# Kernel optimization log

Hardware: AMD Instinct MI355X
Metric: run time of the kernel (lower is better)

## Reference

```python
import jax, jax.numpy as jnp
import numpy as np

D_MODEL = 1024
N_HEADS = 16
N_PHASE = 128              # 8 * n_heads
PHASE_PER_HEAD = N_PHASE // N_HEADS   # 8
HEAD_DIM = D_MODEL // N_HEADS         # 64
B, L = 2, 2048
SCALE = 1.0 / np.sqrt(PHASE_PER_HEAD)
LN_EPS = 1e-5


def _pos_phase(seq_len, n_phase, base=10000.0):
    # RoPE-style frequencies; even and odd columns both carry sinusoid
    inv_freq = 1.0 / base ** (jnp.arange(0, n_phase, 2, dtype=jnp.float32) / n_phase)
    sinusoid = jnp.arange(seq_len, dtype=jnp.float32)[:, None] * inv_freq[None, :]  # (L, n_phase//2)
    return jnp.repeat(sinusoid, 2, axis=1)  # (L, n_phase): cols 0::2 and 1::2 equal sinusoid


def setup_inputs() -> dict:
    key = jax.random.key(0)
    ks = jax.random.split(key, 10)
    xavier = lambda k, shp: jax.random.normal(k, shp, jnp.float32) * np.sqrt(2.0 / (shp[0] + shp[1]))
    return {
        "x_real": jax.random.normal(ks[0], (B, L, D_MODEL), jnp.float32),
        "x_imag": jax.random.normal(ks[1], (B, L, D_MODEL), jnp.float32),
        "Wq": xavier(ks[2], (N_PHASE, D_MODEL)),
        "bq": jax.random.uniform(ks[3], (N_PHASE,), jnp.float32, -np.pi, np.pi),
        "Wk": xavier(ks[4], (N_PHASE, D_MODEL)),
        "bk": jax.random.uniform(ks[5], (N_PHASE,), jnp.float32, -np.pi, np.pi),
        "Wv": xavier(ks[6], (D_MODEL, D_MODEL)),
        "Wo": xavier(ks[7], (D_MODEL, D_MODEL)) / np.sqrt(2.0),
        "gamma": jnp.ones((D_MODEL,), jnp.float32),
        "beta": jnp.zeros((D_MODEL,), jnp.float32),
    }


def reference(x_real, x_imag, Wq, bq, Wk, bk, Wv, Wo, gamma, beta):
    b, l, d = x_real.shape
    pos = _pos_phase(l, N_PHASE)  # (L, n_phase), constant buffer

    # additive phase with position injection
    Qt = (x_imag @ Wq.T + bq + pos).reshape(b, l, N_HEADS, PHASE_PER_HEAD).transpose(0, 2, 1, 3)
    Kt = (x_imag @ Wk.T + bk + pos).reshape(b, l, N_HEADS, PHASE_PER_HEAD).transpose(0, 2, 1, 3)

    # cos(Qi)cos(Kj) + sin(Qi)sin(Kj) as one contraction over stacked features
    qf = jnp.concatenate([jnp.cos(Qt), jnp.sin(Qt)], axis=-1)  # (B,H,L,2P)
    kf = jnp.concatenate([jnp.cos(Kt), jnp.sin(Kt)], axis=-1)
    scores = jnp.einsum('bhip,bhjp->bhij', qf, kf) * SCALE     # (B,H,L,L)

    causal = jnp.triu(jnp.ones((l, l), dtype=bool), 1)
    scores = jnp.where(causal, -jnp.inf, scores)
    attn = jax.nn.softmax(scores, axis=-1)

    V = (x_real @ Wv.T).reshape(b, l, N_HEADS, HEAD_DIM).transpose(0, 2, 1, 3)  # (B,H,L,hd)
    out = jnp.einsum('bhij,bhjd->bhid', attn, V)
    out = out.transpose(0, 2, 1, 3).reshape(b, l, d) @ Wo.T

    # residual + LayerNorm (eps matches torch default)
    h = x_real + out
    mu = jnp.mean(h, axis=-1, keepdims=True)
    var = jnp.mean(jnp.square(h - mu), axis=-1, keepdims=True)
    out_real = (h - mu) * jax.lax.rsqrt(var + LN_EPS) * gamma + beta
    return (out_real, x_imag)
```

## Files before the change

### kernel.cpp

```cpp
#include <hip/hip_runtime.h>
#include <math.h>

#define D_MODEL 1024
#define N_HEADS 16
#define N_PHASE 128
#define HEAD_DIM 64
#define B_SZ 2
#define L_SEQ 2048
#define QK_SCALE 0.35355339059327373f
#define LN_EPS 1e-5f
#define POS_COEF 0.07195578415606394f
#define INV_2PI 0.15915494309189535f

typedef __attribute__((ext_vector_type(8))) short bf16x8;
typedef __attribute__((ext_vector_type(4))) short s16x4;
typedef __attribute__((ext_vector_type(4))) float f32x4;

__device__ __forceinline__ float wave_reduce_sum(float v) {
#pragma unroll
  for (int off = 32; off > 0; off >>= 1) v += __shfl_xor(v, off);
  return v;
}
__device__ __forceinline__ unsigned short f2bf(float x) {
  unsigned u = __float_as_uint(x);
  u += 0x7fffu + ((u >> 16) & 1u);
  return (unsigned short)(u >> 16);
}
__device__ __forceinline__ void gload16(const short* g, short* l) {
  __builtin_amdgcn_global_load_lds(
      (const __attribute__((address_space(1))) void*)g,
      (__attribute__((address_space(3))) void*)l, 16, 0, 0);
}
__device__ __forceinline__ void fast_sincos(float ang, float* s, float* c) {
  float rev = ang * INV_2PI;
  rev = rev - rintf(rev);
  *c = __builtin_amdgcn_cosf(rev);
  *s = __builtin_amdgcn_sinf(rev);
}

#define NX4 ((B_SZ * L_SEQ * D_MODEL) / 4)
#define NWP4 ((N_PHASE * D_MODEL) / 4)
#define NW4 ((D_MODEL * D_MODEL) / 4)
__device__ __forceinline__ s16x4 cvt4(float4 v) {
  s16x4 o;
  o[0] = (short)f2bf(v.x);
  o[1] = (short)f2bf(v.y);
  o[2] = (short)f2bf(v.z);
  o[3] = (short)f2bf(v.w);
  return o;
}
__global__ __launch_bounds__(256) void cvtall_kernel(
    const float* __restrict__ x_real, const float* __restrict__ x_imag,
    const float* __restrict__ Wq, const float* __restrict__ Wk,
    const float* __restrict__ Wv, const float* __restrict__ Wo,
    short* __restrict__ xr_bf, short* __restrict__ xi_bf,
    short* __restrict__ Wq_bf, short* __restrict__ Wk_bf,
    short* __restrict__ Wv_bf, short* __restrict__ Wo_bf,
    float* __restrict__ outi) {
  const int i = blockIdx.x * 256 + threadIdx.x;
  if (i < NX4) {
    const float4 vi = ((const float4*)x_imag)[i];
    ((float4*)outi)[i] = vi;
    ((s16x4*)xi_bf)[i] = cvt4(vi);
    ((s16x4*)xr_bf)[i] = cvt4(((const float4*)x_real)[i]);
  } else if (i < NX4 + NWP4) {
    const int j = i - NX4;
    ((s16x4*)Wq_bf)[j] = cvt4(((const float4*)Wq)[j]);
    ((s16x4*)Wk_bf)[j] = cvt4(((const float4*)Wk)[j]);
  } else if (i < NX4 + NWP4 + NW4) {
    const int j = i - NX4 - NWP4;
    ((s16x4*)Wv_bf)[j] = cvt4(((const float4*)Wv)[j]);
    ((s16x4*)Wo_bf)[j] = cvt4(((const float4*)Wo)[j]);
  }
}

__device__ __forceinline__ void gemm_core(const short* __restrict__ A,
                                          const short* __restrict__ Bm, int K,
                                          int mBase, int nBase,
                                          f32x4 acc[4][2], short* As,
                                          short* Bs) {
  const int tid = threadIdx.x;
  const int wv = tid >> 6, ln = tid & 63;
  const int wr = wv >> 1, wc = wv & 1;
  const int fr = ln & 15, fc = ln >> 4;
  const int cg = (ln & 3) ^ ((ln >> 3) & 3);
  const short* ga = A + (size_t)(mBase + wv * 16 + (ln >> 2)) * K + cg * 8;
  const short* gb = Bm + (size_t)(nBase + wv * 16 + (ln >> 2)) * K + cg * 8;
  short* la = As + wv * 512;
  short* lb = Bs + wv * 512;
  const int ra = (wr * 64 + fr) * 32 + (fc ^ ((fr >> 1) & 3)) * 8;
  const int rb = (wc * 32 + fr) * 32 + (fc ^ ((fr >> 1) & 3)) * 8;

  for (int k0 = 0; k0 < K; k0 += 32) {
    __syncthreads();
    gload16(ga + k0, la);
    gload16(ga + k0 + (size_t)64 * K, la + 64 * 32);
    gload16(gb + k0, lb);
    __syncthreads();

    bf16x8 af[4], bfr[2];
#pragma unroll
    for (int mi = 0; mi < 4; ++mi) af[mi] = *(const bf16x8*)&As[ra + mi * 512];
#pragma unroll
    for (int ni = 0; ni < 2; ++ni) bfr[ni] = *(const bf16x8*)&Bs[rb + ni * 512];

#pragma unroll
    for (int mi = 0; mi < 4; ++mi)
#pragma unroll
      for (int ni = 0; ni < 2; ++ni)
        acc[mi][ni] = __builtin_amdgcn_mfma_f32_16x16x32_bf16(
            af[mi], bfr[ni], acc[mi][ni], 0, 0, 0);
  }
}

__global__ __launch_bounds__(256) void qkv_kernel(
    const short* __restrict__ xi, const short* __restrict__ xr,
    const short* __restrict__ WqB, const short* __restrict__ WkB,
    const short* __restrict__ WvB, const float* __restrict__ bq,
    const float* __restrict__ bk, short* __restrict__ qf,
    short* __restrict__ kf, short* __restrict__ Vt) {
  __shared__ short As[128 * 32];
  __shared__ short Bs[64 * 32];
  const int y = blockIdx.y;
  const int mBase = blockIdx.x * 128;
  const short* A;
  const short* Bm;
  int nBase;
  if (y < 4) {
    A = xi;
    Bm = (y < 2) ? WqB : WkB;
    nBase = (y & 1) * 64;
  } else {
    A = xr;
    Bm = WvB;
    nBase = (y - 4) * 64;
  }

  f32x4 acc[4][2];
#pragma unroll
  for (int i = 0; i < 4; ++i)
#pragma unroll
    for (int j = 0; j < 2; ++j) acc[i][j] = (f32x4){0.f, 0.f, 0.f, 0.f};
  gemm_core(A, Bm, D_MODEL, mBase, nBase, acc, As, Bs);

  const int ln = threadIdx.x & 63, wv = threadIdx.x >> 6;
  const int wr = wv >> 1, wc = wv & 1;
  const int fr = ln & 15, fc = ln >> 4;

  if (y < 4) {
    const float* bias = (y < 2) ? bq : bk;
    short* Cs = (y < 2) ? qf : kf;
    const float fscale = (y < 2) ? QK_SCALE : 1.0f;
#pragma unroll
    for (int mi = 0; mi < 4; ++mi)
#pragma unroll
      for (int ni = 0; ni < 2; ++ni)
#pragma unroll
        for (int r = 0; r < 4; ++r) {
          const int m = mBase + wr * 64 + mi * 16 + fc * 4 + r;
          const int n = nBase + wc * 32 + ni * 16 + fr;
          const int b = m >> 11, l = m & (L_SEQ - 1);
          const float inv_freq = __expf(-(float)(n & ~1) * POS_COEF);
          const float ang = acc[mi][ni][r] + bias[n] + (float)l * inv_freq;
          float sv, cv;
          fast_sincos(ang, &sv, &cv);
          const int h = n >> 3, p = n & 7;
          const size_t base = ((size_t)((b << 4) + h) * L_SEQ + l) * 16;
          Cs[base + p] = (short)f2bf(cv * fscale);
          Cs[base + 8 + p] = (short)f2bf(sv * fscale);
        }
  } else {
#pragma unroll
    for (int mi = 0; mi < 4; ++mi)
#pragma unroll
      for (int ni = 0; ni < 2; ++ni) {
        const int n = nBase + wc * 32 + ni * 16 + fr;
        const int m = mBase + wr * 64 + mi * 16 + fc * 4;
        const int b = m >> 11, l = m & (L_SEQ - 1);
        const int t = (l >> 2) & 7;
        const int tp = ((t << 1) & 6) | (t >> 2);
        const int lpos = (l & ~31) | (tp << 2);
        const int h = n >> 6, d = n & 63;
        const int jc = lpos >> 5, jlo = lpos & 31;
        const int gg = jlo >> 3, ee = jlo & 7;
        s16x4 pk;
#pragma unroll
        for (int r = 0; r < 4; ++r) pk[r] = (short)f2bf(acc[mi][ni][r]);
        const size_t off = (size_t)((b << 4) + h) * 64 * L_SEQ +
                           (size_t)(jc * 4 + (d >> 4)) * 512 + gg * 128 +
                           (d & 15) * 8 + ee;
        *(s16x4*)&Vt[off] = pk;
      }
  }
}

__global__ __launch_bounds__(256) void ogemm_kernel(
    const short* __restrict__ A, const short* __restrict__ Bm,
    const float* __restrict__ resid, float* __restrict__ Cf) {
  __shared__ short As[128 * 32];
  __shared__ short Bs[64 * 32];
  const int mBase = blockIdx.x * 128, nBase = blockIdx.y * 64;

  f32x4 acc[4][2];
#pragma unroll
  for (int i = 0; i < 4; ++i)
#pragma unroll
    for (int j = 0; j < 2; ++j) acc[i][j] = (f32x4){0.f, 0.f, 0.f, 0.f};
  gemm_core(A, Bm, D_MODEL, mBase, nBase, acc, As, Bs);

  const int ln = threadIdx.x & 63, wv = threadIdx.x >> 6;
  const int wr = wv >> 1, wc = wv & 1;
  const int fr = ln & 15, fc = ln >> 4;
#pragma unroll
  for (int mi = 0; mi < 4; ++mi)
#pragma unroll
    for (int ni = 0; ni < 2; ++ni)
#pragma unroll
      for (int r = 0; r < 4; ++r) {
        const int m = mBase + wr * 64 + mi * 16 + fc * 4 + r;
        const int n = nBase + wc * 32 + ni * 16 + fr;
        const size_t idx = (size_t)m * D_MODEL + n;
        Cf[idx] = acc[mi][ni][r] + resid[idx];
      }
}

__global__ __launch_bounds__(256) void attn_mfma_kernel(
    const short* __restrict__ qf, const short* __restrict__ kf,
    const short* __restrict__ Vt, short* __restrict__ ao) {
  const int bh = blockIdx.x;
  const int qg = 127 - (int)blockIdx.y;
  const int tid = threadIdx.x;
  const int w = tid >> 6;
  const int lane = tid & 63;
  const int g = lane >> 4;
  const int q16 = lane & 15;
  const int qglob = qg * 16 + q16;
  const int ntiles = (qg >> 2) + 1;

  __shared__ float ol[4][16][68];
  __shared__ float ll[4][16];

  const short* qf_h = qf + (size_t)bh * L_SEQ * 16;
  const short* kf_h = kf + (size_t)bh * L_SEQ * 16;
  const short* Vt_h = Vt + (size_t)bh * 64 * L_SEQ;
  const int b = bh >> 4, h = bh & 15;

  bf16x8 qfrag = {0, 0, 0, 0, 0, 0, 0, 0};
  if (g < 2) qfrag = *(const bf16x8*)(qf_h + (size_t)qglob * 16 + g * 8);

  f32x4 o[4];
#pragma unroll
  for (int dc = 0; dc < 4; ++dc) o[dc] = (f32x4){0.f, 0.f, 0.f, 0.f};
  float lsum = 0.f;

#pragma unroll 1
  for (int t = w; t < ntiles; t += 4) {
    const int j0 = t << 6;

    bf16x8 vf0[4], vf1[4];
#pragma unroll
    for (int dc = 0; dc < 4; ++dc)
      vf0[dc] = *(const bf16x8*)(Vt_h + ((size_t)((2 * t) * 4 + dc) << 9) +
                                 lane * 8);

    bf16x8 kfr[4];
#pragma unroll
    for (int jt = 0; jt < 4; ++jt) {
      kfr[jt] = (bf16x8){0, 0, 0, 0, 0, 0, 0, 0};
      if (g < 2)
        kfr[jt] =
            *(const bf16x8*)(kf_h + (size_t)(j0 + jt * 16 + q16) * 16 + g * 8);
    }

    f32x4 s[4];
#pragma unroll
    for (int jt = 0; jt < 4; ++jt)
      s[jt] = __builtin_amdgcn_mfma_f32_16x16x32_bf16(
          kfr[jt], qfrag, (f32x4){0.f, 0.f, 0.f, 0.f}, 0, 0, 0);

#pragma unroll
    for (int dc = 0; dc < 4; ++dc)
      vf1[dc] = *(const bf16x8*)(Vt_h + ((size_t)((2 * t + 1) * 4 + dc) << 9) +
                                 lane * 8);

    if (t == ntiles - 1) {
#pragma unroll
      for (int jt = 0; jt < 4; ++jt)
#pragma unroll
        for (int r = 0; r < 4; ++r)
          if (j0 + jt * 16 + g * 4 + r > qglob) s[jt][r] = -INFINITY;
    }

    float ex[4][4];
#pragma unroll
    for (int jt = 0; jt < 4; ++jt)
#pragma unroll
      for (int r = 0; r < 4; ++r) {
        ex[jt][r] = __expf(s[jt][r]);
        lsum += ex[jt][r];
      }

#pragma unroll
    for (int c = 0; c < 2; ++c) {
      union {
        unsigned u[4];
        bf16x8 v;
      } pb;
#pragma unroll
      for (int hw = 0; hw < 2; ++hw) {
        asm("v_cvt_pk_bf16_f32 %0, %1, %2"
            : "=v"(pb.u[hw * 2 + 0])
            : "v"(ex[2 * c + hw][0]), "v"(ex[2 * c + hw][1]));
        asm("v_cvt_pk_bf16_f32 %0, %1, %2"
            : "=v"(pb.u[hw * 2 + 1])
            : "v"(ex[2 * c + hw][2]), "v"(ex[2 * c + hw][3]));
      }
      const bf16x8* vfc = c ? vf1 : vf0;
#pragma unroll
      for (int dc = 0; dc < 4; ++dc)
        o[dc] = __builtin_amdgcn_mfma_f32_16x16x32_bf16(vfc[dc], pb.v, o[dc],
                                                        0, 0, 0);
    }
  }

  lsum += __shfl_xor(lsum, 16);
  lsum += __shfl_xor(lsum, 32);
  if (g == 0) ll[w][q16] = lsum;
#pragma unroll
  for (int dc = 0; dc < 4; ++dc)
    *(f32x4*)&ol[w][q16][dc * 16 + g * 4] = o[dc];
  __syncthreads();

  const float lt = (ll[0][q16] + ll[1][q16]) + (ll[2][q16] + ll[3][q16]);
  const float inv = 1.f / lt;
  const int d0 = w * 16 + g * 4;
  s16x4 pk;
#pragma unroll
  for (int r = 0; r < 4; ++r) {
    const float v = ((ol[0][q16][d0 + r] + ol[1][q16][d0 + r]) +
                     (ol[2][q16][d0 + r] + ol[3][q16][d0 + r]));
    pk[r] = (short)f2bf(v * inv);
  }
  short* orow = ao + ((size_t)(b * L_SEQ + qglob)) * D_MODEL + h * 64;
  *(s16x4*)&orow[d0] = pk;
}

__global__ __launch_bounds__(256) void ln_kernel(float* __restrict__ io,
                                                 const float* __restrict__ gamma,
                                                 const float* __restrict__ beta) {
  const int row = blockIdx.x;
  float* p = io + (size_t)row * D_MODEL;
  const int tid = threadIdx.x;
  float4 x = ((const float4*)p)[tid];
  float s = x.x + x.y + x.z + x.w;
  float sq = x.x * x.x + x.y * x.y + x.z * x.z + x.w * x.w;
  s = wave_reduce_sum(s);
  sq = wave_reduce_sum(sq);
  __shared__ float ss[4], ssq[4];
  const int w = tid >> 6, lane = tid & 63;
  if (lane == 0) {
    ss[w] = s;
    ssq[w] = sq;
  }
  __syncthreads();
  s = ss[0] + ss[1] + ss[2] + ss[3];
  sq = ssq[0] + ssq[1] + ssq[2] + ssq[3];
  const float mean = s * (1.f / D_MODEL);
  const float var = sq * (1.f / D_MODEL) - mean * mean;
  const float rstd = rsqrtf(var + LN_EPS);
  const float4 g = ((const float4*)gamma)[tid];
  const float4 bt = ((const float4*)beta)[tid];
  float4 y;
  y.x = (x.x - mean) * rstd * g.x + bt.x;
  y.y = (x.y - mean) * rstd * g.y + bt.y;
  y.z = (x.z - mean) * rstd * g.z + bt.z;
  y.w = (x.w - mean) * rstd * g.w + bt.w;
  ((float4*)p)[tid] = y;
}

extern "C" void kernel_launch(void* const* d_in, const int* in_sizes, int n_in,
                              void* d_out, int out_size, void* d_ws,
                              size_t ws_size, hipStream_t stream) {
  const float* x_real = (const float*)d_in[0];
  const float* x_imag = (const float*)d_in[1];
  const float* Wq = (const float*)d_in[2];
  const float* bq = (const float*)d_in[3];
  const float* Wk = (const float*)d_in[4];
  const float* bk = (const float*)d_in[5];
  const float* Wv = (const float*)d_in[6];
  const float* Wo = (const float*)d_in[7];
  const float* gamma = (const float*)d_in[8];
  const float* beta = (const float*)d_in[9];

  const size_t n_x = (size_t)B_SZ * L_SEQ * D_MODEL;
  const size_t n_w = (size_t)D_MODEL * D_MODEL;
  const size_t n_wp = (size_t)N_PHASE * D_MODEL;
  const size_t n_qf = (size_t)B_SZ * N_HEADS * L_SEQ * 16;

  short* xi_bf = (short*)d_ws;
  short* xr_bf = xi_bf + n_x;
  short* Wq_bf = xr_bf + n_x;
  short* Wk_bf = Wq_bf + n_wp;
  short* Wv_bf = Wk_bf + n_wp;
  short* Wo_bf = Wv_bf + n_w;
  short* qf = Wo_bf + n_w;
  short* kf = qf + n_qf;
  short* Vt = kf + n_qf;
  short* ao_bf = xr_bf;

  float* outr = (float*)d_out;
  float* outi = outr + n_x;

  const dim3 blk(256);
  const int M = B_SZ * L_SEQ;

  const int cvt_blocks = (NX4 + NWP4 + NW4 + 255) / 256;
  cvtall_kernel<<<dim3(cvt_blocks), blk, 0, stream>>>(
      x_real, x_imag, Wq, Wk, Wv, Wo, xr_bf, xi_bf, Wq_bf, Wk_bf, Wv_bf,
      Wo_bf, outi);

  qkv_kernel<<<dim3(M / 128, 20), blk, 0, stream>>>(
      xi_bf, xr_bf, Wq_bf, Wk_bf, Wv_bf, bq, bk, qf, kf, Vt);
  attn_mfma_kernel<<<dim3(B_SZ * N_HEADS, 128), blk, 0, stream>>>(qf, kf, Vt,
                                                                  ao_bf);
  ogemm_kernel<<<dim3(M / 128, D_MODEL / 64), blk, 0, stream>>>(
      ao_bf, Wo_bf, x_real, outr);
  ln_kernel<<<dim3(M), blk, 0, stream>>>(outr, gamma, beta);
}
```

Baseline: 98.23 us.

## Double the GEMM K-tile to 64 and prefetch next attention tile's K/V

```diff
diff --git a/kernel.cpp b/kernel.cpp
--- a/kernel.cpp
+++ b/kernel.cpp
@@ -83,33 +83,45 @@
   const int wv = tid >> 6, ln = tid & 63;
   const int wr = wv >> 1, wc = wv & 1;
   const int fr = ln & 15, fc = ln >> 4;
-  const int cg = (ln & 3) ^ ((ln >> 3) & 3);
-  const short* ga = A + (size_t)(mBase + wv * 16 + (ln >> 2)) * K + cg * 8;
-  const short* gb = Bm + (size_t)(nBase + wv * 16 + (ln >> 2)) * K + cg * 8;
-  short* la = As + wv * 512;
-  short* lb = Bs + wv * 512;
-  const int ra = (wr * 64 + fr) * 32 + (fc ^ ((fr >> 1) & 3)) * 8;
-  const int rb = (wc * 32 + fr) * 32 + (fc ^ ((fr >> 1) & 3)) * 8;
-
-  for (int k0 = 0; k0 < K; k0 += 32) {
+  const int row8 = ln >> 3;
+  const int cg = (ln & 7) ^ row8;
+  const short* ga = A + (size_t)(mBase + wv * 32 + row8) * K + cg * 8;
+  const short* gb = Bm + (size_t)(nBase + wv * 16 + row8) * K + cg * 8;
+  short* la = As + wv * 2048;
+  short* lb = Bs + wv * 1024;
+  const int swz = fr & 7;
+
+  for (int k0 = 0; k0 < K; k0 += 64) {
     __syncthreads();
-    gload16(ga + k0, la);
-    gload16(ga + k0 + (size_t)64 * K, la + 64 * 32);
-    gload16(gb + k0, lb);
+#pragma unroll
+    for (int i = 0; i < 4; ++i)
+      gload16(ga + k0 + (size_t)(8 * i) * K, la + i * 512);
+#pragma unroll
+    for (int i = 0; i < 2; ++i)
+      gload16(gb + k0 + (size_t)(8 * i) * K, lb + i * 512);
     __syncthreads();
 
-    bf16x8 af[4], bfr[2];
-#pragma unroll
-    for (int mi = 0; mi < 4; ++mi) af[mi] = *(const bf16x8*)&As[ra + mi * 512];
-#pragma unroll
-    for (int ni = 0; ni < 2; ++ni) bfr[ni] = *(const bf16x8*)&Bs[rb + ni * 512];
-
-#pragma unroll
-    for (int mi = 0; mi < 4; ++mi)
+    bf16x8 af[2][4], bfr[2][2];
+#pragma unroll
+    for (int kk = 0; kk < 2; ++kk) {
+      const int pc = ((kk * 4 + fc) ^ swz) * 8;
+#pragma unroll
+      for (int mi = 0; mi < 4; ++mi)
+        af[kk][mi] =
+            *(const bf16x8*)&As[(wr * 64 + mi * 16 + fr) * 64 + pc];
 #pragma unroll
       for (int ni = 0; ni < 2; ++ni)
-        acc[mi][ni] = __builtin_amdgcn_mfma_f32_16x16x32_bf16(
-            af[mi], bfr[ni], acc[mi][ni], 0, 0, 0);
+        bfr[kk][ni] =
+            *(const bf16x8*)&Bs[(wc * 32 + ni * 16 + fr) * 64 + pc];
+    }
+#pragma unroll
+    for (int kk = 0; kk < 2; ++kk)
+#pragma unroll
+      for (int mi = 0; mi < 4; ++mi)
+#pragma unroll
+        for (int ni = 0; ni < 2; ++ni)
+          acc[mi][ni] = __builtin_amdgcn_mfma_f32_16x16x32_bf16(
+              af[kk][mi], bfr[kk][ni], acc[mi][ni], 0, 0, 0);
   }
 }
 
@@ -119,8 +131,8 @@
     const short* __restrict__ WvB, const float* __restrict__ bq,
     const float* __restrict__ bk, short* __restrict__ qf,
     short* __restrict__ kf, short* __restrict__ Vt) {
-  __shared__ short As[128 * 32];
-  __shared__ short Bs[64 * 32];
+  __shared__ short As[128 * 64];
+  __shared__ short Bs[64 * 64];
   const int y = blockIdx.y;
   const int mBase = blockIdx.x * 128;
   const short* A;
@@ -197,8 +209,8 @@
 __global__ __launch_bounds__(256) void ogemm_kernel(
     const short* __restrict__ A, const short* __restrict__ Bm,
     const float* __restrict__ resid, float* __restrict__ Cf) {
-  __shared__ short As[128 * 32];
-  __shared__ short Bs[64 * 32];
+  __shared__ short As[128 * 64];
+  __shared__ short Bs[64 * 64];
   const int mBase = blockIdx.x * 128, nBase = blockIdx.y * 64;
 
   f32x4 acc[4][2];
@@ -253,35 +265,62 @@
   for (int dc = 0; dc < 4; ++dc) o[dc] = (f32x4){0.f, 0.f, 0.f, 0.f};
   float lsum = 0.f;
 
+  bf16x8 vA[4], vB[4], kc[4];
+#pragma unroll
+  for (int jt = 0; jt < 4; ++jt) kc[jt] = (bf16x8){0, 0, 0, 0, 0, 0, 0, 0};
+  if (w < ntiles) {
+#pragma unroll
+    for (int dc = 0; dc < 4; ++dc) {
+      vA[dc] = *(const bf16x8*)(Vt_h + ((size_t)((2 * w) * 4 + dc) << 9) +
+                                lane * 8);
+      vB[dc] = *(const bf16x8*)(Vt_h + ((size_t)((2 * w + 1) * 4 + dc) << 9) +
+                                lane * 8);
+    }
+    if (g < 2) {
+#pragma unroll
+      for (int jt = 0; jt < 4; ++jt)
+        kc[jt] = *(const bf16x8*)(kf_h +
+                                  (size_t)((w << 6) + jt * 16 + q16) * 16 +
+                                  g * 8);
+    }
+  }
+
 #pragma unroll 1
   for (int t = w; t < ntiles; t += 4) {
     const int j0 = t << 6;
-
-    bf16x8 vf0[4], vf1[4];
-#pragma unroll
-    for (int dc = 0; dc < 4; ++dc)
-      vf0[dc] = *(const bf16x8*)(Vt_h + ((size_t)((2 * t) * 4 + dc) << 9) +
-                                 lane * 8);
-
-    bf16x8 kfr[4];
-#pragma unroll
-    for (int jt = 0; jt < 4; ++jt) {
-      kfr[jt] = (bf16x8){0, 0, 0, 0, 0, 0, 0, 0};
-      if (g < 2)
-        kfr[jt] =
-            *(const bf16x8*)(kf_h + (size_t)(j0 + jt * 16 + q16) * 16 + g * 8);
+    const int tn = t + 4;
+
+    bf16x8 vAn[4], vBn[4], kn[4];
+#pragma unroll
+    for (int jt = 0; jt < 4; ++jt) kn[jt] = kc[jt];
+#pragma unroll
+    for (int dc = 0; dc < 4; ++dc) {
+      vAn[dc] = vA[dc];
+      vBn[dc] = vB[dc];
+    }
+    if (tn < ntiles) {
+#pragma unroll
+      for (int dc = 0; dc < 4; ++dc) {
+        vAn[dc] = *(const bf16x8*)(Vt_h + ((size_t)((2 * tn) * 4 + dc) << 9) +
+                                   lane * 8);
+        vBn[dc] = *(const bf16x8*)(Vt_h +
+                                   ((size_t)((2 * tn + 1) * 4 + dc) << 9) +
+                                   lane * 8);
+      }
+      if (g < 2) {
+#pragma unroll
+        for (int jt = 0; jt < 4; ++jt)
+          kn[jt] = *(const bf16x8*)(kf_h +
+                                    (size_t)((tn << 6) + jt * 16 + q16) * 16 +
+                                    g * 8);
+      }
     }
 
     f32x4 s[4];
 #pragma unroll
     for (int jt = 0; jt < 4; ++jt)
       s[jt] = __builtin_amdgcn_mfma_f32_16x16x32_bf16(
-          kfr[jt], qfrag, (f32x4){0.f, 0.f, 0.f, 0.f}, 0, 0, 0);
-
-#pragma unroll
-    for (int dc = 0; dc < 4; ++dc)
-      vf1[dc] = *(const bf16x8*)(Vt_h + ((size_t)((2 * t + 1) * 4 + dc) << 9) +
-                                 lane * 8);
+          kc[jt], qfrag, (f32x4){0.f, 0.f, 0.f, 0.f}, 0, 0, 0);
 
     if (t == ntiles - 1) {
 #pragma unroll
@@ -315,11 +354,19 @@
             : "=v"(pb.u[hw * 2 + 1])
             : "v"(ex[2 * c + hw][2]), "v"(ex[2 * c + hw][3]));
       }
-      const bf16x8* vfc = c ? vf1 : vf0;
+      const bf16x8* vfc = c ? vB : vA;
 #pragma unroll
       for (int dc = 0; dc < 4; ++dc)
         o[dc] = __builtin_amdgcn_mfma_f32_16x16x32_bf16(vfc[dc], pb.v, o[dc],
                                                         0, 0, 0);
+    }
+
+#pragma unroll
+    for (int jt = 0; jt < 4; ++jt) kc[jt] = kn[jt];
+#pragma unroll
+    for (int dc = 0; dc < 4; ++dc) {
+      vA[dc] = vAn[dc];
+      vB[dc] = vBn[dc];
     }
   }
 
```

Result: faster. 95.83 us (-2.4%).
